# Kernel optimization log

Measured on AMD Instinct MI355X. Metric: run time of the kernel, lower is better.

Reference implementation:

```python
import jax, jax.numpy as jnp
import numpy as np

DIM = 1024
HEADS = 16
MLP = 4096
EPS = 1e-5

def _layer_norm(x, g, b):
    mu = jnp.mean(x, axis=-1, keepdims=True)
    var = jnp.mean(jnp.square(x - mu), axis=-1, keepdims=True)
    return (x - mu) * jax.lax.rsqrt(var + EPS) * g + b

def setup_inputs() -> dict:
    key = jax.random.key(0)
    ks = jax.random.split(key, 8)
    s = 0.02
    return {
        "x": jax.random.normal(ks[0], (2, 2048, DIM), dtype=jnp.float32),
        "ln1_g": jnp.ones((DIM,), jnp.float32),
        "ln1_b": jnp.zeros((DIM,), jnp.float32),
        "qkv_w": jax.random.normal(ks[1], (DIM, 3 * DIM), jnp.float32) * s,
        "qkv_b": jnp.zeros((3 * DIM,), jnp.float32),
        "proj_w": jax.random.normal(ks[2], (DIM, DIM), jnp.float32) * s,
        "proj_b": jnp.zeros((DIM,), jnp.float32),
        "ln2_g": jnp.ones((DIM,), jnp.float32),
        "ln2_b": jnp.zeros((DIM,), jnp.float32),
        "fc1_w": jax.random.normal(ks[3], (DIM, MLP), jnp.float32) * s,
        "fc1_b": jnp.zeros((MLP,), jnp.float32),
        "fc2_w": jax.random.normal(ks[4], (MLP, DIM), jnp.float32) * s,
        "fc2_b": jnp.zeros((DIM,), jnp.float32),
    }

def reference(x, ln1_g, ln1_b, qkv_w, qkv_b, proj_w, proj_b,
              ln2_g, ln2_b, fc1_w, fc1_b, fc2_w, fc2_b):
    B, N, C = x.shape
    H = HEADS
    D = C // H
    # --- attention (pre-norm); NOTE: source applies no 1/sqrt(D) scaling ---
    h = _layer_norm(x, ln1_g, ln1_b)
    qkv = (h @ qkv_w + qkv_b).reshape(B, N, 3, H, D)
    q, k, v = (qkv[:, :, 0], qkv[:, :, 1], qkv[:, :, 2])  # [B,N,H,D]
    qk = jnp.einsum('bnhd,bmhd->bhnm', q, k)
    attn = jax.nn.softmax(qk, axis=-1)
    y = jnp.einsum('bhnm,bmhd->bnhd', attn, v).reshape(B, N, C)
    y = y @ proj_w + proj_b
    x = x + y
    # --- MLP (pre-norm), exact GELU like torch nn.GELU ---
    h2 = _layer_norm(x, ln2_g, ln2_b)
    h2 = jax.nn.gelu(h2 @ fc1_w + fc1_b, approximate=False)
    x = x + (h2 @ fc2_w + fc2_b)
    return x
```

## Files before the change

kernel.cpp:

```cpp
#include <hip/hip_runtime.h>
#include <hip/hip_bf16.h>

#define CDIM   1024
#define NSEQ   2048
#define NHEAD  16
#define HDIM   64
#define MLPDIM 4096
#define TROWS  4096

typedef __attribute__((ext_vector_type(8)))  __bf16 bf16x8;
typedef __attribute__((ext_vector_type(4)))  float  f32x4;
typedef __attribute__((ext_vector_type(16))) float  f32x16;
typedef __attribute__((ext_vector_type(4)))  unsigned short us4;

static __device__ __forceinline__ unsigned short f2bf(float f) {
  unsigned int u = __float_as_uint(f);
  u += 0x7fffu + ((u >> 16) & 1u);
  return (unsigned short)(u >> 16);
}

#define MFMA16(a, b, c) __builtin_amdgcn_mfma_f32_16x16x32_bf16(a, b, c, 0, 0, 0)
#define MFMA32(a, b, c) __builtin_amdgcn_mfma_f32_32x32x16_bf16(a, b, c, 0, 0, 0)

static __device__ __forceinline__ void gll16(const unsigned short* g, unsigned short* l) {
  __builtin_amdgcn_global_load_lds(
      (const __attribute__((address_space(1))) unsigned int*)g,
      (__attribute__((address_space(3))) unsigned int*)l, 16, 0, 0);
}

__global__ __launch_bounds__(256)
void ln_bf16_kernel(const float* __restrict__ x,
                    const float* __restrict__ gam,
                    const float* __restrict__ bet,
                    unsigned short* __restrict__ out)
{
  int row = blockIdx.x;
  int t = threadIdx.x;
  const float4* xr = (const float4*)(x + (size_t)row * CDIM);
  float4 v = xr[t];
  float s  = v.x + v.y + v.z + v.w;
  float s2 = v.x*v.x + v.y*v.y + v.z*v.z + v.w*v.w;
  #pragma unroll
  for (int off = 32; off > 0; off >>= 1) {
    s  += __shfl_down(s, off);
    s2 += __shfl_down(s2, off);
  }
  __shared__ float rs[4], rs2[4];
  int wave = t >> 6, lane = t & 63;
  if (lane == 0) { rs[wave] = s; rs2[wave] = s2; }
  __syncthreads();
  float fs  = rs[0] + rs[1] + rs[2] + rs[3];
  float fs2 = rs2[0] + rs2[1] + rs2[2] + rs2[3];
  float mu   = fs * (1.0f / CDIM);
  float var  = fs2 * (1.0f / CDIM) - mu * mu;
  float rstd = rsqrtf(var + 1e-5f);
  float4 gg = ((const float4*)gam)[t];
  float4 bb = ((const float4*)bet)[t];
  us4 o;
  o.x = f2bf((v.x - mu) * rstd * gg.x + bb.x);
  o.y = f2bf((v.y - mu) * rstd * gg.y + bb.y);
  o.z = f2bf((v.z - mu) * rstd * gg.z + bb.z);
  o.w = f2bf((v.w - mu) * rstd * gg.w + bb.w);
  ((us4*)(out + (size_t)row * CDIM))[t] = o;
}

__global__ __launch_bounds__(256)
void wt_bf16_kernel(const float* __restrict__ W, unsigned short* __restrict__ Wt,
                    int K, int N)
{
  __shared__ float tile[32][33];
  int n0 = blockIdx.x * 32, k0 = blockIdx.y * 32;
  int t = threadIdx.x;
  int r = t >> 3, c4 = (t & 7) << 2;
  float4 v = *(const float4*)(W + (size_t)(k0 + r) * N + n0 + c4);
  tile[r][c4 + 0] = v.x; tile[r][c4 + 1] = v.y;
  tile[r][c4 + 2] = v.z; tile[r][c4 + 3] = v.w;
  __syncthreads();
  us4 o;
  o.x = f2bf(tile[c4 + 0][r]);
  o.y = f2bf(tile[c4 + 1][r]);
  o.z = f2bf(tile[c4 + 2][r]);
  o.w = f2bf(tile[c4 + 3][r]);
  *(us4*)(Wt + (size_t)(n0 + r) * K + k0 + c4) = o;
}

template<int EPI>
__global__ __launch_bounds__(256, 4)
void gemm_bt(const unsigned short* __restrict__ A, const unsigned short* __restrict__ Bt,
             const float* __restrict__ bias, int M, int N, int K,
             float* __restrict__ outf, unsigned short* __restrict__ outb,
             const float* __restrict__ resid,
             unsigned short* __restrict__ qo, unsigned short* __restrict__ ko,
             unsigned short* __restrict__ vo)
{
  __shared__ unsigned short As[2][128 * 32];
  __shared__ unsigned short Bs[2][128 * 32];
  const int tid  = threadIdx.x;
  const int lane = tid & 63;
  const int wave = tid >> 6;
  const int wr = wave >> 1, wc = wave & 1;
  const int g = lane >> 4, r16 = lane & 15;
  const int bm = blockIdx.y * 128, bn = blockIdx.x * 128;

  auto stage = [&](int d, int k0) {
    #pragma unroll
    for (int c = 0; c < 2; c++) {
      int o   = (c * 256 + tid) << 3;
      int row = o >> 5;
      int col = o & 31;
      int ub  = (c * 256 + (tid & ~63)) << 3;
      gll16(A  + (size_t)(bm + row) * K + k0 + col, &As[d][ub]);
      gll16(Bt + (size_t)(bn + row) * K + k0 + col, &Bs[d][ub]);
    }
  };

  f32x4 acc[4][4];
  #pragma unroll
  for (int i = 0; i < 4; i++)
    #pragma unroll
    for (int j = 0; j < 4; j++) acc[i][j] = (f32x4){0.f, 0.f, 0.f, 0.f};

  stage(0, 0);
  const int nkt = K / 32;
  for (int kt = 0; kt < nkt; kt++) {
    const int cur = kt & 1;
    __syncthreads();
    if (kt + 1 < nkt) stage(cur ^ 1, (kt + 1) * 32);
    bf16x8 af[4], bfr[4];
    #pragma unroll
    for (int i = 0; i < 4; i++) {
      int row = wr * 64 + i * 16 + r16;
      af[i] = *(const bf16x8*)(&As[cur][row * 32 + 8 * g]);
    }
    #pragma unroll
    for (int j = 0; j < 4; j++) {
      int row = wc * 64 + j * 16 + r16;
      bfr[j] = *(const bf16x8*)(&Bs[cur][row * 32 + 8 * g]);
    }
    __builtin_amdgcn_s_setprio(1);
    #pragma unroll
    for (int i = 0; i < 4; i++)
      #pragma unroll
      for (int j = 0; j < 4; j++)
        acc[i][j] = MFMA16(af[i], bfr[j], acc[i][j]);
    __builtin_amdgcn_s_setprio(0);
  }

  #pragma unroll
  for (int i = 0; i < 4; i++) {
    #pragma unroll
    for (int j = 0; j < 4; j++) {
      int col = bn + wc * 64 + j * 16 + r16;
      float bv = bias[col];
      #pragma unroll
      for (int jj = 0; jj < 4; jj++) {
        int row = bm + wr * 64 + i * 16 + 4 * g + jj;
        float val = acc[i][j][jj] + bv;
        if (EPI == 1) {
          int sel = col >> 10, cc = col & 1023;
          int hh = cc >> 6, d = cc & 63;
          int b = row >> 11, tk = row & 2047;
          size_t hb = (size_t)(b * NHEAD + hh);
          if (sel == 0)      qo[(hb * NSEQ + tk) * HDIM + d] = f2bf(val * 1.4426950408889634f);
          else if (sel == 1) ko[(hb * NSEQ + tk) * HDIM + d] = f2bf(val);
          else               vo[(hb * HDIM + d) * NSEQ + tk] = f2bf(val);
        } else if (EPI == 2) {
          size_t idx = (size_t)row * N + col;
          outf[idx] = val + resid[idx];
        } else {
          float ge = 0.5f * val * (1.0f + erff(val * 0.70710678118654752f));
          outb[(size_t)row * N + col] = f2bf(ge);
        }
      }
    }
  }
}

__global__ __launch_bounds__(256, 2)
void attn_kernel(const unsigned short* __restrict__ q, const unsigned short* __restrict__ k,
                 const unsigned short* __restrict__ vt, unsigned short* __restrict__ y)
{
  int bid = blockIdx.x;
  int xcd = bid & 7, loc = bid >> 3;
  int bh  = xcd * 4 + (loc >> 4);
  int qchunk = loc & 15;
  int b = bh >> 4, h = bh & 15;
  int wave = threadIdx.x >> 6, lane = threadIdx.x & 63;
  int ql = lane & 31;
  int hi = lane >> 5;
  int q0 = qchunk * 128 + wave * 32;
  const unsigned short* qb = q  + (size_t)bh * NSEQ * HDIM;
  const unsigned short* kb = k  + (size_t)bh * NSEQ * HDIM;
  const unsigned short* vb = vt + (size_t)bh * HDIM * NSEQ;

  __shared__ unsigned short KL[2][2048];
  __shared__ unsigned short VL[2][2048];

  auto stage = [&](int d, int it) {
    int kv0 = it * 32;
    {
      int c = wave * 64 + lane;
      int row = c >> 3, col = c & 7;
      int sc  = (row << 3) | (col ^ (row & 7));
      gll16(kb + (size_t)kv0 * HDIM + sc * 8, &KL[d][wave * 512]);
    }
    {
      int c = wave * 64 + lane;
      int row = c >> 2, col = c & 3;
      int scol = col ^ ((row >> 1) & 3);
      gll16(vb + (size_t)row * NSEQ + kv0 + scol * 8, &VL[d][wave * 512]);
    }
  };

  bf16x8 aq[4];
  #pragma unroll
  for (int s = 0; s < 4; s++)
    aq[s] = *(const bf16x8*)(qb + (size_t)(q0 + ql) * HDIM + s * 16 + hi * 8);

  float m = -1e30f, ssum = 0.f;
  f32x16 o0, o1;
  #pragma unroll
  for (int r = 0; r < 16; r++) { o0[r] = 0.f; o1[r] = 0.f; }

  stage(0, 0);
  for (int it = 0; it < NSEQ / 32; it++) {
    const int cur = it & 1;
    __syncthreads();
    if (it + 1 < NSEQ / 32) stage(cur ^ 1, it + 1);
    bf16x8 kf[4];
    #pragma unroll
    for (int s = 0; s < 4; s++)
      kf[s] = *(const bf16x8*)((const char*)KL[cur] +
               ql * 128 + ((((s << 1) | hi) ^ (ql & 7)) << 4));
    f32x16 sacc;
    #pragma unroll
    for (int r = 0; r < 16; r++) sacc[r] = 0.f;
    __builtin_amdgcn_s_setprio(1);
    #pragma unroll
    for (int s = 0; s < 4; s++)
      sacc = MFMA32(kf[s], aq[s], sacc);
    __builtin_amdgcn_s_setprio(0);
    float tmax = sacc[0];
    #pragma unroll
    for (int r = 1; r < 16; r++) tmax = fmaxf(tmax, sacc[r]);
    tmax = fmaxf(tmax, __shfl_xor(tmax, 32));
    float mn = fmaxf(m, tmax);
    float scale = exp2f(m - mn);
    m = mn;
    float ps = 0.f;
    #pragma unroll
    for (int r = 0; r < 16; r++) {
      sacc[r] = exp2f(sacc[r] - mn);
      ps += sacc[r];
    }
    ssum = ssum * scale + ps;
    #pragma unroll
    for (int r = 0; r < 16; r++) { o0[r] *= scale; o1[r] *= scale; }
    bf16x8 vf[2][2];
    #pragma unroll
    for (int t = 0; t < 2; t++)
      #pragma unroll
      for (int db = 0; db < 2; db++)
        vf[t][db] = *(const bf16x8*)((const char*)VL[cur] +
                     (db * 32 + ql) * 64 + ((((t << 1) | hi) ^ ((ql >> 1) & 3)) << 4));
    __builtin_amdgcn_s_setprio(1);
    #pragma unroll
    for (int t = 0; t < 2; t++) {
      unsigned pk01, pk23, pk45, pk67;
      asm("v_cvt_pk_bf16_f32 %0, %1, %2" : "=v"(pk01) : "v"(sacc[8*t+0]), "v"(sacc[8*t+1]));
      asm("v_cvt_pk_bf16_f32 %0, %1, %2" : "=v"(pk23) : "v"(sacc[8*t+2]), "v"(sacc[8*t+3]));
      asm("v_cvt_pk_bf16_f32 %0, %1, %2" : "=v"(pk45) : "v"(sacc[8*t+4]), "v"(sacc[8*t+5]));
      asm("v_cvt_pk_bf16_f32 %0, %1, %2" : "=v"(pk67) : "v"(sacc[8*t+6]), "v"(sacc[8*t+7]));
      asm("v_permlane32_swap_b32 %0, %1" : "+v"(pk01), "+v"(pk45));
      asm("v_permlane32_swap_b32 %0, %1" : "+v"(pk23), "+v"(pk67));
      union { unsigned u[4]; bf16x8 v; } pf;
      pf.u[0] = pk01; pf.u[1] = pk23; pf.u[2] = pk45; pf.u[3] = pk67;
      o0 = MFMA32(vf[t][0], pf.v, o0);
      o1 = MFMA32(vf[t][1], pf.v, o1);
    }
    __builtin_amdgcn_s_setprio(0);
  }
  float stot = ssum + __shfl_xor(ssum, 32);
  float inv = 1.0f / stot;
  unsigned short* yr = y + ((size_t)(b * NSEQ + q0 + ql)) * CDIM + h * HDIM;
  #pragma unroll
  for (int db = 0; db < 2; db++) {
    const f32x16& oo = db ? o1 : o0;
    #pragma unroll
    for (int rq = 0; rq < 4; rq++) {
      us4 w;
      w.x = f2bf(oo[4*rq+0] * inv);
      w.y = f2bf(oo[4*rq+1] * inv);
      w.z = f2bf(oo[4*rq+2] * inv);
      w.w = f2bf(oo[4*rq+3] * inv);
      *(us4*)(yr + db * 32 + rq * 8 + hi * 4) = w;
    }
  }
}

extern "C" void kernel_launch(void* const* d_in, const int* in_sizes, int n_in,
                              void* d_out, int out_size, void* d_ws, size_t ws_size,
                              hipStream_t stream)
{
  const float* x      = (const float*)d_in[0];
  const float* ln1_g  = (const float*)d_in[1];
  const float* ln1_b  = (const float*)d_in[2];
  const float* qkv_w  = (const float*)d_in[3];
  const float* qkv_b  = (const float*)d_in[4];
  const float* proj_w = (const float*)d_in[5];
  const float* proj_b = (const float*)d_in[6];
  const float* ln2_g  = (const float*)d_in[7];
  const float* ln2_b  = (const float*)d_in[8];
  const float* fc1_w  = (const float*)d_in[9];
  const float* fc1_b  = (const float*)d_in[10];
  const float* fc2_w  = (const float*)d_in[11];
  const float* fc2_b  = (const float*)d_in[12];
  float* out = (float*)d_out;

  char* p = (char*)d_ws;
  size_t off = 0;
  auto alloc = [&](size_t bytes) -> void* {
    void* r = p + off; off += (bytes + 255) & ~(size_t)255; return r;
  };
  unsigned short* wt_qkv  = (unsigned short*)alloc((size_t)3072 * 1024 * 2);
  unsigned short* wt_proj = (unsigned short*)alloc((size_t)1024 * 1024 * 2);
  unsigned short* wt_fc1  = (unsigned short*)alloc((size_t)4096 * 1024 * 2);
  unsigned short* wt_fc2  = (unsigned short*)alloc((size_t)1024 * 4096 * 2);
  unsigned short* h1  = (unsigned short*)alloc((size_t)TROWS * CDIM * 2);
  unsigned short* qb  = (unsigned short*)alloc((size_t)TROWS * CDIM * 2);
  unsigned short* kb  = (unsigned short*)alloc((size_t)TROWS * CDIM * 2);
  unsigned short* vtb = (unsigned short*)alloc((size_t)TROWS * CDIM * 2);
  unsigned short* yb  = (unsigned short*)alloc((size_t)TROWS * CDIM * 2);
  float*          x1  = (float*)alloc((size_t)TROWS * CDIM * 4);
  unsigned short* h2  = (unsigned short*)alloc((size_t)TROWS * CDIM * 2);
  unsigned short* g1  = (unsigned short*)alloc((size_t)TROWS * MLPDIM * 2);

  dim3 blk(256);
  wt_bf16_kernel<<<dim3(3072 / 32, 1024 / 32), blk, 0, stream>>>(qkv_w, wt_qkv, 1024, 3072);
  wt_bf16_kernel<<<dim3(1024 / 32, 1024 / 32), blk, 0, stream>>>(proj_w, wt_proj, 1024, 1024);
  wt_bf16_kernel<<<dim3(4096 / 32, 1024 / 32), blk, 0, stream>>>(fc1_w, wt_fc1, 1024, 4096);
  wt_bf16_kernel<<<dim3(1024 / 32, 4096 / 32), blk, 0, stream>>>(fc2_w, wt_fc2, 4096, 1024);
  ln_bf16_kernel<<<TROWS, blk, 0, stream>>>(x, ln1_g, ln1_b, h1);
  gemm_bt<1><<<dim3(3072 / 128, TROWS / 128), blk, 0, stream>>>(
      h1, wt_qkv, qkv_b, TROWS, 3072, 1024,
      nullptr, nullptr, nullptr, qb, kb, vtb);
  attn_kernel<<<dim3(512), blk, 0, stream>>>(qb, kb, vtb, yb);
  gemm_bt<2><<<dim3(1024 / 128, TROWS / 128), blk, 0, stream>>>(
      yb, wt_proj, proj_b, TROWS, 1024, 1024,
      x1, nullptr, x, nullptr, nullptr, nullptr);
  ln_bf16_kernel<<<TROWS, blk, 0, stream>>>(x1, ln2_g, ln2_b, h2);
  gemm_bt<3><<<dim3(MLPDIM / 128, TROWS / 128), blk, 0, stream>>>(
      h2, wt_fc1, fc1_b, TROWS, MLPDIM, 1024,
      nullptr, g1, nullptr, nullptr, nullptr, nullptr);
  gemm_bt<2><<<dim3(1024 / 128, TROWS / 128), blk, 0, stream>>>(
      g1, wt_fc2, fc2_b, TROWS, 1024, MLPDIM,
      out, nullptr, x1, nullptr, nullptr, nullptr);
}
```

Baseline: 302.6 us.

## Split-K the fc2 GEMM and remap GEMM workgroups across XCDs

Linearizes the GEMM grid and remaps block IDs so consecutive tiles land on the same XCD, which should improve L2 reuse. It also splits the fc2 GEMM (K=4096) into two K halves to double its workgroup count from 256 to 512. The second half writes partial sums to a scratch buffer that aliases the freed q buffer, and an extra add kernel folds them into the output. This adds an extra fp32 write/read pass over the output and another kernel launch, in exchange for better occupancy on the long-K GEMM.

```diff
diff --git a/kernel.cpp b/kernel.cpp
--- a/kernel.cpp
+++ b/kernel.cpp
@@ -87,9 +87,9 @@
 template<int EPI>
 __global__ __launch_bounds__(256, 4)
 void gemm_bt(const unsigned short* __restrict__ A, const unsigned short* __restrict__ Bt,
-             const float* __restrict__ bias, int M, int N, int K,
+             const float* __restrict__ bias, int Kstride, int Kc, int nbx, int nby,
              float* __restrict__ outf, unsigned short* __restrict__ outb,
-             const float* __restrict__ resid,
+             const float* __restrict__ resid, float* __restrict__ pp,
              unsigned short* __restrict__ qo, unsigned short* __restrict__ ko,
              unsigned short* __restrict__ vo)
 {
@@ -100,7 +100,16 @@
   const int wave = tid >> 6;
   const int wr = wave >> 1, wc = wave & 1;
   const int g = lane >> 4, r16 = lane & 15;
-  const int bm = blockIdx.y * 128, bn = blockIdx.x * 128;
+
+  const int nwg = gridDim.x;
+  const int orig = ((int)blockIdx.x & 7) * (nwg >> 3) + ((int)blockIdx.x >> 3);
+  const int bx = orig % nbx;
+  const int t2 = orig / nbx;
+  const int by = t2 % nby;
+  const int kz = t2 / nby;
+  const int bm = by * 128, bn = bx * 128;
+  const int kbase = kz * Kc;
+  const int N = nbx * 128;
 
   auto stage = [&](int d, int k0) {
     #pragma unroll
@@ -109,8 +118,8 @@
       int row = o >> 5;
       int col = o & 31;
       int ub  = (c * 256 + (tid & ~63)) << 3;
-      gll16(A  + (size_t)(bm + row) * K + k0 + col, &As[d][ub]);
-      gll16(Bt + (size_t)(bn + row) * K + k0 + col, &Bs[d][ub]);
+      gll16(A  + (size_t)(bm + row) * Kstride + kbase + k0 + col, &As[d][ub]);
+      gll16(Bt + (size_t)(bn + row) * Kstride + kbase + k0 + col, &Bs[d][ub]);
     }
   };
 
@@ -121,7 +130,7 @@
     for (int j = 0; j < 4; j++) acc[i][j] = (f32x4){0.f, 0.f, 0.f, 0.f};
 
   stage(0, 0);
-  const int nkt = K / 32;
+  const int nkt = Kc / 32;
   for (int kt = 0; kt < nkt; kt++) {
     const int cur = kt & 1;
     __syncthreads();
@@ -151,7 +160,7 @@
     #pragma unroll
     for (int j = 0; j < 4; j++) {
       int col = bn + wc * 64 + j * 16 + r16;
-      float bv = bias[col];
+      float bv = (EPI == 2 && kz != 0) ? 0.f : bias[col];
       #pragma unroll
       for (int jj = 0; jj < 4; jj++) {
         int row = bm + wr * 64 + i * 16 + 4 * g + jj;
@@ -166,13 +175,27 @@
           else               vo[(hb * HDIM + d) * NSEQ + tk] = f2bf(val);
         } else if (EPI == 2) {
           size_t idx = (size_t)row * N + col;
-          outf[idx] = val + resid[idx];
+          if (kz == 0) outf[idx] = val + resid[idx];
+          else         pp[idx]   = val;
         } else {
           float ge = 0.5f * val * (1.0f + erff(val * 0.70710678118654752f));
           outb[(size_t)row * N + col] = f2bf(ge);
         }
       }
     }
+  }
+}
+
+__global__ __launch_bounds__(256)
+void add_kernel(float* __restrict__ out, const float* __restrict__ pp, int n4)
+{
+  int i = blockIdx.x * 256 + threadIdx.x;
+  int stride = gridDim.x * 256;
+  for (; i < n4; i += stride) {
+    float4 a = ((const float4*)out)[i];
+    float4 b = ((const float4*)pp)[i];
+    a.x += b.x; a.y += b.y; a.z += b.z; a.w += b.w;
+    ((float4*)out)[i] = a;
   }
 }
 
@@ -334,6 +357,7 @@
   float*          x1  = (float*)alloc((size_t)TROWS * CDIM * 4);
   unsigned short* h2  = (unsigned short*)alloc((size_t)TROWS * CDIM * 2);
   unsigned short* g1  = (unsigned short*)alloc((size_t)TROWS * MLPDIM * 2);
+  float* pp = (float*)qb;
 
   dim3 blk(256);
   wt_bf16_kernel<<<dim3(3072 / 32, 1024 / 32), blk, 0, stream>>>(qkv_w, wt_qkv, 1024, 3072);
@@ -341,18 +365,19 @@
   wt_bf16_kernel<<<dim3(4096 / 32, 1024 / 32), blk, 0, stream>>>(fc1_w, wt_fc1, 1024, 4096);
   wt_bf16_kernel<<<dim3(1024 / 32, 4096 / 32), blk, 0, stream>>>(fc2_w, wt_fc2, 4096, 1024);
   ln_bf16_kernel<<<TROWS, blk, 0, stream>>>(x, ln1_g, ln1_b, h1);
-  gemm_bt<1><<<dim3(3072 / 128, TROWS / 128), blk, 0, stream>>>(
-      h1, wt_qkv, qkv_b, TROWS, 3072, 1024,
-      nullptr, nullptr, nullptr, qb, kb, vtb);
+  gemm_bt<1><<<dim3(768), blk, 0, stream>>>(
+      h1, wt_qkv, qkv_b, 1024, 1024, 24, 32,
+      nullptr, nullptr, nullptr, nullptr, qb, kb, vtb);
   attn_kernel<<<dim3(512), blk, 0, stream>>>(qb, kb, vtb, yb);
-  gemm_bt<2><<<dim3(1024 / 128, TROWS / 128), blk, 0, stream>>>(
-      yb, wt_proj, proj_b, TROWS, 1024, 1024,
-      x1, nullptr, x, nullptr, nullptr, nullptr);
+  gemm_bt<2><<<dim3(256), blk, 0, stream>>>(
+      yb, wt_proj, proj_b, 1024, 1024, 8, 32,
+      x1, nullptr, x, nullptr, nullptr, nullptr, nullptr);
   ln_bf16_kernel<<<TROWS, blk, 0, stream>>>(x1, ln2_g, ln2_b, h2);
-  gemm_bt<3><<<dim3(MLPDIM / 128, TROWS / 128), blk, 0, stream>>>(
-      h2, wt_fc1, fc1_b, TROWS, MLPDIM, 1024,
-      nullptr, g1, nullptr, nullptr, nullptr, nullptr);
-  gemm_bt<2><<<dim3(1024 / 128, TROWS / 128), blk, 0, stream>>>(
-      g1, wt_fc2, fc2_b, TROWS, 1024, MLPDIM,
-      out, nullptr, x1, nullptr, nullptr, nullptr);
-}
+  gemm_bt<3><<<dim3(1024), blk, 0, stream>>>(
+      h2, wt_fc1, fc1_b, 1024, 1024, 32, 32,
+      nullptr, g1, nullptr, nullptr, nullptr, nullptr, nullptr);
+  gemm_bt<2><<<dim3(512), blk, 0, stream>>>(
+      g1, wt_fc2, fc2_b, 4096, 2048, 8, 32,
+      out, nullptr, x1, pp, nullptr, nullptr, nullptr);
+  add_kernel<<<dim3(2048), blk, 0, stream>>>(out, pp, TROWS * CDIM / 4);
+}
```

Result: no change. 304.2 us (+0.5%).
